# Kernel optimization log

Hardware: AMD Instinct MI355X
Metric: run time of the kernel (lower is better)

## Reference

```python
import jax, jax.numpy as jnp
import numpy as np

DIM = 128
HEADS = 4
DIM_HEAD = 32
NUM_MEM = 4
H = 256
W = 256
SCALE = DIM_HEAD ** -0.5
NORM_SCALE = DIM ** 0.5


def rms_norm(x, gamma):
    # x: (c, h, w); L2-normalize over channel axis, per spatial location
    x32 = x.astype(jnp.float32)
    n = jnp.linalg.norm(x32, ord=2, axis=0)  # (h, w)
    return (x32 / n * (gamma + 1.0) * NORM_SCALE).astype(x.dtype)


def setup_inputs() -> dict:
    key = jax.random.key(0)
    k0, k1, k2, k3 = jax.random.split(key, 4)
    x = jax.random.normal(k0, (DIM, H, W), dtype=jnp.float32)
    gamma1 = jnp.zeros((DIM, 1, 1), dtype=jnp.float32)
    w_qkv = jax.random.normal(k1, (3 * HEADS * DIM_HEAD, DIM), dtype=jnp.float32) * 0.05
    mem_kv = jax.random.normal(k2, (2, HEADS, DIM_HEAD, NUM_MEM), dtype=jnp.float32)
    w_out = jax.random.normal(k3, (DIM, HEADS * DIM_HEAD), dtype=jnp.float32) * 0.05
    b_out = jnp.zeros((DIM,), dtype=jnp.float32)
    gamma2 = jnp.zeros((DIM, 1, 1), dtype=jnp.float32)
    return {"x": x, "gamma1": gamma1, "w_qkv": w_qkv, "mem_kv": mem_kv,
            "w_out": w_out, "b_out": b_out, "gamma2": gamma2}


def reference(x, gamma1, w_qkv, mem_kv, w_out, b_out, gamma2):
    n = H * W
    xn = rms_norm(x, gamma1)
    # 1x1 conv == channel matmul: (3*hid, c) @ (c, h*w)
    qkv = jnp.einsum('oc,cn->on', w_qkv, xn.reshape(DIM, n))
    q, k, v = jnp.split(qkv, 3, axis=0)
    # (h*d, n) -> (h, d, n)
    q = q.reshape(HEADS, DIM_HEAD, n)
    k = k.reshape(HEADS, DIM_HEAD, n)
    v = v.reshape(HEADS, DIM_HEAD, n)
    mk, mv = mem_kv[0], mem_kv[1]  # (h, d, num_mem)
    k = jnp.concatenate([mk, k], axis=-1)  # (h, d, num_mem + n)
    v = jnp.concatenate([mv, v], axis=-1)
    # softmax over feature dim for q (global max subtract), token dim for k
    q = jax.nn.softmax((q - jnp.max(q)).astype(jnp.float32), axis=-2).astype(q.dtype)
    k = jax.nn.softmax((k - jnp.max(k)).astype(jnp.float32), axis=-1).astype(k.dtype)
    q = q * SCALE
    context = jnp.einsum('hdn,hen->hde', k, v)      # (h, d, d)
    out = jnp.einsum('hde,hdn->hen', context, q)    # (h, d, n)
    out = out.reshape(HEADS * DIM_HEAD, H, W)
    out = jnp.einsum('oc,chw->ohw', w_out, out) + b_out[:, None, None]
    return rms_norm(out, gamma2)
```

## Files before the change

### kernel.cpp

```cpp
#include <hip/hip_runtime.h>
#include <hip/hip_bf16.h>
#include <cstddef>


typedef __attribute__((ext_vector_type(8))) short short8;
typedef __attribute__((ext_vector_type(4))) float f32x4;

static constexpr int   NTOK = 65536;
static constexpr float NORM_SCALE_F = 11.313708498984761f;
static constexpr float SCALE_F      = 0.17677669529663687f;

__device__ __forceinline__ unsigned short f2bf(float f) {
  __hip_bfloat16 h = __float2bfloat16(f);
  return *reinterpret_cast<unsigned short*>(&h);
}

__global__ __launch_bounds__(256) void k0_pack(const float* __restrict__ w_qkv,
                                               const float* __restrict__ gamma1,
                                               unsigned short* __restrict__ Wp) {
  const int id = blockIdx.x * 256 + threadIdx.x;
  const int m = id / 16384, p = id % 16384;
  const int j = p & 7, ln = (p >> 3) & 63, frag = p >> 9;
  const int ks = frag & 3, rt = frag >> 2;
  const int row = rt * 16 + (ln & 15);
  const int c = ks * 32 + (ln >> 4) * 8 + j;
  const float v = w_qkv[(m * 128 + row) * 128 + c] * (gamma1[c] + 1.0f) * NORM_SCALE_F;
  Wp[id] = f2bf(v);
}

__global__ __launch_bounds__(512) void k1_kv(const float* __restrict__ x,
                                             const unsigned short* __restrict__ Wkp,
                                             const unsigned short* __restrict__ Wvp,
                                             float* __restrict__ Cp,
                                             float* __restrict__ Sp) {
  __shared__ unsigned short kvs[8][2560];
  const int tid = threadIdx.x, wv = tid >> 6, ln = tid & 63;
  const int g4 = ln >> 4, t16 = ln & 15;
  const int n0 = (blockIdx.x * 8 + wv) * 32;
  unsigned short* keb = &kvs[wv][0];
  unsigned short* vb  = &kvs[wv][1280];

  short8 xf[2][4];
  float scn[2];
  #pragma unroll
  for (int tg = 0; tg < 2; ++tg) {
    float sq = 0.f;
    #pragma unroll
    for (int ks = 0; ks < 4; ++ks) {
      short8 v;
      #pragma unroll
      for (int j = 0; j < 8; ++j) {
        const float f = x[(size_t)(ks * 32 + g4 * 8 + j) * NTOK + n0 + tg * 16 + t16];
        sq += f * f;
        v[j] = (short)f2bf(f);
      }
      xf[tg][ks] = v;
    }
    sq += __shfl_xor(sq, 16, 64);
    sq += __shfl_xor(sq, 32, 64);
    scn[tg] = rsqrtf(sq);
  }

  f32x4 cacc[4][2][2] = {};
  float sacc[4][2][4] = {};

  #pragma unroll
  for (int h = 0; h < 4; ++h) {
    f32x4 ka[2][2] = {};
    #pragma unroll
    for (int ks = 0; ks < 4; ++ks) {
      const short8 a0 = *reinterpret_cast<const short8*>(Wkp + (((2 * h + 0) * 4 + ks) * 64 + ln) * 8);
      const short8 a1 = *reinterpret_cast<const short8*>(Wkp + (((2 * h + 1) * 4 + ks) * 64 + ln) * 8);
      #pragma unroll
      for (int tg = 0; tg < 2; ++tg) {
        ka[0][tg] = __builtin_amdgcn_mfma_f32_16x16x32_bf16(a0, xf[tg][ks], ka[0][tg], 0, 0, 0);
        ka[1][tg] = __builtin_amdgcn_mfma_f32_16x16x32_bf16(a1, xf[tg][ks], ka[1][tg], 0, 0, 0);
      }
    }
    #pragma unroll
    for (int rtl = 0; rtl < 2; ++rtl)
      #pragma unroll
      for (int tg = 0; tg < 2; ++tg)
        #pragma unroll
        for (int r = 0; r < 4; ++r) {
          const float ke = __expf(ka[rtl][tg][r] * scn[tg]);
          sacc[h][rtl][r] += ke;
          keb[(rtl * 16 + g4 * 4 + r) * 40 + tg * 16 + t16] = f2bf(ke);
        }
    f32x4 va[2][2] = {};
    #pragma unroll
    for (int ks = 0; ks < 4; ++ks) {
      const short8 a0 = *reinterpret_cast<const short8*>(Wvp + (((2 * h + 0) * 4 + ks) * 64 + ln) * 8);
      const short8 a1 = *reinterpret_cast<const short8*>(Wvp + (((2 * h + 1) * 4 + ks) * 64 + ln) * 8);
      #pragma unroll
      for (int tg = 0; tg < 2; ++tg) {
        va[0][tg] = __builtin_amdgcn_mfma_f32_16x16x32_bf16(a0, xf[tg][ks], va[0][tg], 0, 0, 0);
        va[1][tg] = __builtin_amdgcn_mfma_f32_16x16x32_bf16(a1, xf[tg][ks], va[1][tg], 0, 0, 0);
      }
    }
    #pragma unroll
    for (int rtl = 0; rtl < 2; ++rtl)
      #pragma unroll
      for (int tg = 0; tg < 2; ++tg)
        #pragma unroll
        for (int r = 0; r < 4; ++r)
          vb[(rtl * 16 + g4 * 4 + r) * 40 + tg * 16 + t16] = f2bf(va[rtl][tg][r] * scn[tg]);

    asm volatile("s_waitcnt lgkmcnt(0)" ::: "memory");
    short8 keA[2], vB[2];
    #pragma unroll
    for (int dt = 0; dt < 2; ++dt)
      keA[dt] = *reinterpret_cast<const short8*>(keb + (dt * 16 + t16) * 40 + g4 * 8);
    #pragma unroll
    for (int et = 0; et < 2; ++et)
      vB[et] = *reinterpret_cast<const short8*>(vb + (et * 16 + t16) * 40 + g4 * 8);
    #pragma unroll
    for (int dt = 0; dt < 2; ++dt)
      #pragma unroll
      for (int et = 0; et < 2; ++et)
        cacc[h][dt][et] = __builtin_amdgcn_mfma_f32_16x16x32_bf16(keA[dt], vB[et], cacc[h][dt][et], 0, 0, 0);
    asm volatile("s_waitcnt lgkmcnt(0)" ::: "memory");
  }

  #pragma unroll
  for (int h = 0; h < 4; ++h)
    #pragma unroll
    for (int rtl = 0; rtl < 2; ++rtl)
      #pragma unroll
      for (int r = 0; r < 4; ++r) {
        float s = sacc[h][rtl][r];
        s += __shfl_xor(s, 1, 64);
        s += __shfl_xor(s, 2, 64);
        s += __shfl_xor(s, 4, 64);
        s += __shfl_xor(s, 8, 64);
        sacc[h][rtl][r] = s;
      }

  __syncthreads();
  float* cred = reinterpret_cast<float*>(&kvs[0][0]);
  for (int w = 0; w < 8; ++w) {
    if (wv == w) {
      #pragma unroll
      for (int h = 0; h < 4; ++h)
        #pragma unroll
        for (int dt = 0; dt < 2; ++dt)
          #pragma unroll
          for (int et = 0; et < 2; ++et)
            #pragma unroll
            for (int r = 0; r < 4; ++r) {
              const int idx = h * 1024 + (dt * 16 + g4 * 4 + r) * 32 + et * 16 + t16;
              if (w == 0) cred[idx] = cacc[h][dt][et][r];
              else        cred[idx] += cacc[h][dt][et][r];
            }
      if (t16 == 0) {
        #pragma unroll
        for (int h = 0; h < 4; ++h)
          #pragma unroll
          for (int rtl = 0; rtl < 2; ++rtl)
            #pragma unroll
            for (int r = 0; r < 4; ++r) {
              const int si = 4096 + h * 32 + rtl * 16 + g4 * 4 + r;
              if (w == 0) cred[si] = sacc[h][rtl][r];
              else        cred[si] += sacc[h][rtl][r];
            }
      }
    }
    __syncthreads();
  }
  for (int i = tid; i < 4096; i += 512)
    Cp[(size_t)blockIdx.x * 4096 + i] = cred[i];
  if (tid < 128)
    Sp[blockIdx.x * 128 + tid] = cred[4096 + tid];
}

__global__ __launch_bounds__(256) void k3a_reduce(const float* __restrict__ Cp,
                                                  const float* __restrict__ Sp,
                                                  float* __restrict__ Cpp) {
  __shared__ float red[256];
  const int t = threadIdx.x;
  const int eg = blockIdx.x;
  const int ch = blockIdx.y;
  const int e = eg * 128 + (t & 127);
  const int half = t >> 7;
  float s = 0.f;
  for (int bb = 0; bb < 16; ++bb) {
    const int b = ch * 32 + half * 16 + bb;
    s += (e < 4096) ? Cp[(size_t)b * 4096 + e] : Sp[b * 128 + (e - 4096)];
  }
  red[t] = s;
  __syncthreads();
  if (t < 128) Cpp[ch * 4224 + eg * 128 + t] = red[t] + red[t + 128];
}

__global__ __launch_bounds__(256) void k3b1_ctx(const float* __restrict__ Cpp,
                                                const float* __restrict__ mem_kv,
                                                float* __restrict__ ctx) {
  __shared__ float allv[4224];
  const int t = threadIdx.x;
  for (int e = t; e < 4224; e += 256) {
    float s = 0.f;
    #pragma unroll
    for (int c = 0; c < 8; ++c) s += Cpp[c * 4224 + e];
    allv[e] = s;
  }
  __syncthreads();
  for (int e = t; e < 4224; e += 256) {
    if (e < 4096) {
      const int hh = e >> 10, d = (e >> 5) & 31, ev = e & 31;
      float add = 0.f;
      #pragma unroll
      for (int m = 0; m < 4; ++m)
        add += __expf(mem_kv[(hh * 32 + d) * 4 + m]) * mem_kv[512 + (hh * 32 + ev) * 4 + m];
      allv[e] += add;
    } else {
      const int si = e - 4096;
      const int hh = si >> 5, d = si & 31;
      float add = 0.f;
      #pragma unroll
      for (int m = 0; m < 4; ++m) add += __expf(mem_kv[(hh * 32 + d) * 4 + m]);
      allv[e] += add;
    }
  }
  __syncthreads();
  for (int e = t; e < 4096; e += 256)
    ctx[e] = allv[e] / allv[4096 + (e >> 5)];
}

__global__ __launch_bounds__(256) void k3b2_w2(const float* __restrict__ ctx,
                                               const float* __restrict__ w_out,
                                               unsigned short* __restrict__ W2p) {
  const int t = threadIdx.x;
  const int hd = t & 127;
  const int og = t >> 7;
  const int hh = hd >> 5, d = hd & 31;
  const int bo = blockIdx.x;
  #pragma unroll
  for (int i = 0; i < 8; ++i) {
    const int o = bo * 16 + og * 8 + i;
    float s = 0.f;
    #pragma unroll
    for (int e = 0; e < 32; ++e)
      s += w_out[o * 128 + hh * 32 + e] * ctx[hh * 1024 + d * 32 + e];
    const int rt = o >> 4, ks = hd >> 5;
    const int lnp = ((hd & 31) >> 3) * 16 + (o & 15);
    const int j = hd & 7;
    W2p[((rt * 4 + ks) * 64 + lnp) * 8 + j] = f2bf(s * SCALE_F);
  }
}

__global__ __launch_bounds__(512) void k5_out(const float* __restrict__ x,
                                              const unsigned short* __restrict__ Wqp,
                                              const unsigned short* __restrict__ W2p,
                                              const float* __restrict__ b_out,
                                              const float* __restrict__ gamma2,
                                              float* __restrict__ y) {
  __shared__ unsigned short qs[8][4096];
  const int tid = threadIdx.x, wv = tid >> 6, ln = tid & 63;
  const int g4 = ln >> 4, t16 = ln & 15;
  const int n0 = (blockIdx.x * 8 + wv) * 32;
  unsigned short* qb_lds = &qs[wv][0];

  short8 xf[2][4];
  float scn[2];
  #pragma unroll
  for (int tg = 0; tg < 2; ++tg) {
    float sq = 0.f;
    #pragma unroll
    for (int ks = 0; ks < 4; ++ks) {
      short8 v;
      #pragma unroll
      for (int j = 0; j < 8; ++j) {
        const float f = x[(size_t)(ks * 32 + g4 * 8 + j) * NTOK + n0 + tg * 16 + t16];
        sq += f * f;
        v[j] = (short)f2bf(f);
      }
      xf[tg][ks] = v;
    }
    sq += __shfl_xor(sq, 16, 64);
    sq += __shfl_xor(sq, 32, 64);
    scn[tg] = rsqrtf(sq);
  }

  #pragma unroll
  for (int h = 0; h < 4; ++h) {
    f32x4 qa[2][2] = {};
    #pragma unroll
    for (int ks = 0; ks < 4; ++ks) {
      const short8 a0 = *reinterpret_cast<const short8*>(Wqp + (((2 * h + 0) * 4 + ks) * 64 + ln) * 8);
      const short8 a1 = *reinterpret_cast<const short8*>(Wqp + (((2 * h + 1) * 4 + ks) * 64 + ln) * 8);
      #pragma unroll
      for (int tg = 0; tg < 2; ++tg) {
        qa[0][tg] = __builtin_amdgcn_mfma_f32_16x16x32_bf16(a0, xf[tg][ks], qa[0][tg], 0, 0, 0);
        qa[1][tg] = __builtin_amdgcn_mfma_f32_16x16x32_bf16(a1, xf[tg][ks], qa[1][tg], 0, 0, 0);
      }
    }
    #pragma unroll
    for (int tg = 0; tg < 2; ++tg) {
      float ev[2][4];
      float s = 0.f;
      #pragma unroll
      for (int rtl = 0; rtl < 2; ++rtl)
        #pragma unroll
        for (int r = 0; r < 4; ++r) {
          ev[rtl][r] = __expf(qa[rtl][tg][r] * scn[tg]);
          s += ev[rtl][r];
        }
      s += __shfl_xor(s, 16, 64);
      s += __shfl_xor(s, 32, 64);
      const float inv = 1.0f / s;
      #pragma unroll
      for (int rtl = 0; rtl < 2; ++rtl)
        #pragma unroll
        for (int r = 0; r < 4; ++r)
          qa[rtl][tg][r] = ev[rtl][r] * inv;
    }
    #pragma unroll
    for (int rtl = 0; rtl < 2; ++rtl) {
      const int rt = 2 * h + rtl;
      #pragma unroll
      for (int tg = 0; tg < 2; ++tg) {
        ushort4 w4;
        w4.x = f2bf(qa[rtl][tg][0]);
        w4.y = f2bf(qa[rtl][tg][1]);
        w4.z = f2bf(qa[rtl][tg][2]);
        w4.w = f2bf(qa[rtl][tg][3]);
        const int idxb = ((tg * 4 + (rt >> 1)) * 64 + ((rt & 1) * 2 + (g4 >> 1)) * 16 + t16) * 8 + (g4 & 1) * 4;
        *reinterpret_cast<ushort4*>(&qb_lds[idxb]) = w4;
      }
    }
  }

  asm volatile("s_waitcnt lgkmcnt(0)" ::: "memory");

  short8 qb[2][4];
  #pragma unroll
  for (int tg = 0; tg < 2; ++tg)
    #pragma unroll
    for (int ks = 0; ks < 4; ++ks)
      qb[tg][ks] = *reinterpret_cast<const short8*>(&qb_lds[((tg * 4 + ks) * 64 + ln) * 8]);

  f32x4 z[8][2] = {};
  #pragma unroll
  for (int ks = 0; ks < 4; ++ks)
    #pragma unroll
    for (int rt = 0; rt < 8; ++rt) {
      const short8 a = *reinterpret_cast<const short8*>(W2p + ((rt * 4 + ks) * 64 + ln) * 8);
      #pragma unroll
      for (int tg = 0; tg < 2; ++tg)
        z[rt][tg] = __builtin_amdgcn_mfma_f32_16x16x32_bf16(a, qb[tg][ks], z[rt][tg], 0, 0, 0);
    }

  float ssq[2] = {0.f, 0.f};
  #pragma unroll
  for (int rt = 0; rt < 8; ++rt) {
    const float4 bb = *reinterpret_cast<const float4*>(b_out + rt * 16 + g4 * 4);
    const float barr[4] = {bb.x, bb.y, bb.z, bb.w};
    #pragma unroll
    for (int tg = 0; tg < 2; ++tg)
      #pragma unroll
      for (int r = 0; r < 4; ++r) {
        const float zb = z[rt][tg][r] + barr[r];
        z[rt][tg][r] = zb;
        ssq[tg] += zb * zb;
      }
  }
  float rr[2];
  #pragma unroll
  for (int tg = 0; tg < 2; ++tg) {
    float s = ssq[tg];
    s += __shfl_xor(s, 16, 64);
    s += __shfl_xor(s, 32, 64);
    rr[tg] = rsqrtf(s);
  }
  #pragma unroll
  for (int rt = 0; rt < 8; ++rt) {
    const float4 gg = *reinterpret_cast<const float4*>(gamma2 + rt * 16 + g4 * 4);
    const float garr[4] = {gg.x, gg.y, gg.z, gg.w};
    #pragma unroll
    for (int tg = 0; tg < 2; ++tg)
      #pragma unroll
      for (int r = 0; r < 4; ++r) {
        const int row = rt * 16 + g4 * 4 + r;
        y[(size_t)row * NTOK + n0 + tg * 16 + t16] =
            z[rt][tg][r] * rr[tg] * (garr[r] + 1.0f) * NORM_SCALE_F;
      }
  }
}

extern "C" void kernel_launch(void* const* d_in, const int* in_sizes, int n_in,
                              void* d_out, int out_size, void* d_ws, size_t ws_size,
                              hipStream_t stream) {
  const float* x      = (const float*)d_in[0];
  const float* gamma1 = (const float*)d_in[1];
  const float* w_qkv  = (const float*)d_in[2];
  const float* mem_kv = (const float*)d_in[3];
  const float* w_out  = (const float*)d_in[4];
  const float* b_out  = (const float*)d_in[5];
  const float* gamma2 = (const float*)d_in[6];
  float* out = (float*)d_out;
  float* ws  = (float*)d_ws;

  unsigned short* Wqp = (unsigned short*)ws;
  unsigned short* Wkp = Wqp + 16384;
  unsigned short* Wvp = Wkp + 16384;
  unsigned short* W2p = Wvp + 16384;
  float* Cp  = ws + 32768;
  float* Sp  = Cp + 1048576;
  float* Cpp = Sp + 32768;
  float* ctx = Cpp + 33792;

  hipLaunchKernelGGL(k0_pack,  dim3(192),    dim3(256), 0, stream, w_qkv, gamma1, Wqp);
  hipLaunchKernelGGL(k1_kv,    dim3(256),    dim3(512), 0, stream, x, Wkp, Wvp, Cp, Sp);
  hipLaunchKernelGGL(k3a_reduce, dim3(33, 8), dim3(256), 0, stream, Cp, Sp, Cpp);
  hipLaunchKernelGGL(k3b1_ctx, dim3(1),      dim3(256), 0, stream, Cpp, mem_kv, ctx);
  hipLaunchKernelGGL(k3b2_w2,  dim3(8),      dim3(256), 0, stream, ctx, w_out, W2p);
  hipLaunchKernelGGL(k5_out,   dim3(256),    dim3(512), 0, stream, x, Wqp, W2p, b_out, gamma2, out);
}
```

Measured before the change: 204.4 us.

## Swap MFMA operand roles to keep K/V and Q fragments in registers

Swaps the MFMA operand order so the projected K, V and Q tiles come out in the register layout needed as inputs to the next MFMA. This drops the per-wave LDS staging round-trips in both the kv and output kernels. The x normalization moves before the bf16 conversion. Per-block reductions of context and sums now use shared-memory atomics into one combined buffer instead of a serialized per-wave loop. The output kernel is relaunched with 256-thread blocks and no LDS, and the W2 packing writes vectorized fragments. In exchange there is atomic contention on LDS, and applying the norm scale before rounding slightly changes the numerics.

```diff
diff --git a/kernel.cpp b/kernel.cpp
--- a/kernel.cpp
+++ b/kernel.cpp
@@ -14,6 +14,7 @@
   __hip_bfloat16 h = __float2bfloat16(f);
   return *reinterpret_cast<unsigned short*>(&h);
 }
+__device__ __forceinline__ short sbf(float f) { return (short)f2bf(f); }
 
 __global__ __launch_bounds__(256) void k0_pack(const float* __restrict__ w_qkv,
                                                const float* __restrict__ gamma1,
@@ -31,150 +32,111 @@
 __global__ __launch_bounds__(512) void k1_kv(const float* __restrict__ x,
                                              const unsigned short* __restrict__ Wkp,
                                              const unsigned short* __restrict__ Wvp,
-                                             float* __restrict__ Cp,
-                                             float* __restrict__ Sp) {
-  __shared__ unsigned short kvs[8][2560];
+                                             float* __restrict__ CpAll) {
+  __shared__ float cred[4224];
   const int tid = threadIdx.x, wv = tid >> 6, ln = tid & 63;
   const int g4 = ln >> 4, t16 = ln & 15;
   const int n0 = (blockIdx.x * 8 + wv) * 32;
-  unsigned short* keb = &kvs[wv][0];
-  unsigned short* vb  = &kvs[wv][1280];
+
+  for (int i = tid; i < 4224; i += 512) cred[i] = 0.f;
+  __syncthreads();
 
   short8 xf[2][4];
-  float scn[2];
   #pragma unroll
   for (int tg = 0; tg < 2; ++tg) {
+    float tmp[4][8];
     float sq = 0.f;
     #pragma unroll
-    for (int ks = 0; ks < 4; ++ks) {
-      short8 v;
+    for (int ks = 0; ks < 4; ++ks)
       #pragma unroll
       for (int j = 0; j < 8; ++j) {
         const float f = x[(size_t)(ks * 32 + g4 * 8 + j) * NTOK + n0 + tg * 16 + t16];
+        tmp[ks][j] = f;
         sq += f * f;
-        v[j] = (short)f2bf(f);
-      }
-      xf[tg][ks] = v;
-    }
+      }
     sq += __shfl_xor(sq, 16, 64);
     sq += __shfl_xor(sq, 32, 64);
-    scn[tg] = rsqrtf(sq);
-  }
-
-  f32x4 cacc[4][2][2] = {};
-  float sacc[4][2][4] = {};
+    const float s = rsqrtf(sq);
+    #pragma unroll
+    for (int ks = 0; ks < 4; ++ks) {
+      short8 v;
+      #pragma unroll
+      for (int j = 0; j < 8; ++j) v[j] = sbf(tmp[ks][j] * s);
+      xf[tg][ks] = v;
+    }
+  }
 
   #pragma unroll
   for (int h = 0; h < 4; ++h) {
     f32x4 ka[2][2] = {};
     #pragma unroll
     for (int ks = 0; ks < 4; ++ks) {
-      const short8 a0 = *reinterpret_cast<const short8*>(Wkp + (((2 * h + 0) * 4 + ks) * 64 + ln) * 8);
-      const short8 a1 = *reinterpret_cast<const short8*>(Wkp + (((2 * h + 1) * 4 + ks) * 64 + ln) * 8);
+      const short8 b0 = *reinterpret_cast<const short8*>(Wkp + (((2 * h + 0) * 4 + ks) * 64 + ln) * 8);
+      const short8 b1 = *reinterpret_cast<const short8*>(Wkp + (((2 * h + 1) * 4 + ks) * 64 + ln) * 8);
       #pragma unroll
       for (int tg = 0; tg < 2; ++tg) {
-        ka[0][tg] = __builtin_amdgcn_mfma_f32_16x16x32_bf16(a0, xf[tg][ks], ka[0][tg], 0, 0, 0);
-        ka[1][tg] = __builtin_amdgcn_mfma_f32_16x16x32_bf16(a1, xf[tg][ks], ka[1][tg], 0, 0, 0);
-      }
-    }
-    #pragma unroll
-    for (int rtl = 0; rtl < 2; ++rtl)
+        ka[0][tg] = __builtin_amdgcn_mfma_f32_16x16x32_bf16(xf[tg][ks], b0, ka[0][tg], 0, 0, 0);
+        ka[1][tg] = __builtin_amdgcn_mfma_f32_16x16x32_bf16(xf[tg][ks], b1, ka[1][tg], 0, 0, 0);
+      }
+    }
+    short8 keA[2];
+    #pragma unroll
+    for (int mt = 0; mt < 2; ++mt) {
+      float sl = 0.f;
+      short8 u;
       #pragma unroll
       for (int tg = 0; tg < 2; ++tg)
         #pragma unroll
         for (int r = 0; r < 4; ++r) {
-          const float ke = __expf(ka[rtl][tg][r] * scn[tg]);
-          sacc[h][rtl][r] += ke;
-          keb[(rtl * 16 + g4 * 4 + r) * 40 + tg * 16 + t16] = f2bf(ke);
+          const float e = __expf(ka[mt][tg][r]);
+          sl += e;
+          u[tg * 4 + r] = sbf(e);
         }
+      keA[mt] = u;
+      sl += __shfl_xor(sl, 16, 64);
+      sl += __shfl_xor(sl, 32, 64);
+      if (g4 == 0) atomicAdd(&cred[4096 + h * 32 + mt * 16 + t16], sl);
+    }
     f32x4 va[2][2] = {};
     #pragma unroll
     for (int ks = 0; ks < 4; ++ks) {
-      const short8 a0 = *reinterpret_cast<const short8*>(Wvp + (((2 * h + 0) * 4 + ks) * 64 + ln) * 8);
-      const short8 a1 = *reinterpret_cast<const short8*>(Wvp + (((2 * h + 1) * 4 + ks) * 64 + ln) * 8);
+      const short8 b0 = *reinterpret_cast<const short8*>(Wvp + (((2 * h + 0) * 4 + ks) * 64 + ln) * 8);
+      const short8 b1 = *reinterpret_cast<const short8*>(Wvp + (((2 * h + 1) * 4 + ks) * 64 + ln) * 8);
       #pragma unroll
       for (int tg = 0; tg < 2; ++tg) {
-        va[0][tg] = __builtin_amdgcn_mfma_f32_16x16x32_bf16(a0, xf[tg][ks], va[0][tg], 0, 0, 0);
-        va[1][tg] = __builtin_amdgcn_mfma_f32_16x16x32_bf16(a1, xf[tg][ks], va[1][tg], 0, 0, 0);
-      }
-    }
-    #pragma unroll
-    for (int rtl = 0; rtl < 2; ++rtl)
+        va[0][tg] = __builtin_amdgcn_mfma_f32_16x16x32_bf16(xf[tg][ks], b0, va[0][tg], 0, 0, 0);
+        va[1][tg] = __builtin_amdgcn_mfma_f32_16x16x32_bf16(xf[tg][ks], b1, va[1][tg], 0, 0, 0);
+      }
+    }
+    short8 vB[2];
+    #pragma unroll
+    for (int et = 0; et < 2; ++et) {
+      short8 u;
       #pragma unroll
       for (int tg = 0; tg < 2; ++tg)
         #pragma unroll
         for (int r = 0; r < 4; ++r)
-          vb[(rtl * 16 + g4 * 4 + r) * 40 + tg * 16 + t16] = f2bf(va[rtl][tg][r] * scn[tg]);
-
-    asm volatile("s_waitcnt lgkmcnt(0)" ::: "memory");
-    short8 keA[2], vB[2];
+          u[tg * 4 + r] = sbf(va[et][tg][r]);
+      vB[et] = u;
+    }
     #pragma unroll
     for (int dt = 0; dt < 2; ++dt)
-      keA[dt] = *reinterpret_cast<const short8*>(keb + (dt * 16 + t16) * 40 + g4 * 8);
-    #pragma unroll
-    for (int et = 0; et < 2; ++et)
-      vB[et] = *reinterpret_cast<const short8*>(vb + (et * 16 + t16) * 40 + g4 * 8);
-    #pragma unroll
-    for (int dt = 0; dt < 2; ++dt)
-      #pragma unroll
-      for (int et = 0; et < 2; ++et)
-        cacc[h][dt][et] = __builtin_amdgcn_mfma_f32_16x16x32_bf16(keA[dt], vB[et], cacc[h][dt][et], 0, 0, 0);
-    asm volatile("s_waitcnt lgkmcnt(0)" ::: "memory");
-  }
-
-  #pragma unroll
-  for (int h = 0; h < 4; ++h)
-    #pragma unroll
-    for (int rtl = 0; rtl < 2; ++rtl)
-      #pragma unroll
-      for (int r = 0; r < 4; ++r) {
-        float s = sacc[h][rtl][r];
-        s += __shfl_xor(s, 1, 64);
-        s += __shfl_xor(s, 2, 64);
-        s += __shfl_xor(s, 4, 64);
-        s += __shfl_xor(s, 8, 64);
-        sacc[h][rtl][r] = s;
-      }
-
-  __syncthreads();
-  float* cred = reinterpret_cast<float*>(&kvs[0][0]);
-  for (int w = 0; w < 8; ++w) {
-    if (wv == w) {
-      #pragma unroll
-      for (int h = 0; h < 4; ++h)
-        #pragma unroll
-        for (int dt = 0; dt < 2; ++dt)
-          #pragma unroll
-          for (int et = 0; et < 2; ++et)
-            #pragma unroll
-            for (int r = 0; r < 4; ++r) {
-              const int idx = h * 1024 + (dt * 16 + g4 * 4 + r) * 32 + et * 16 + t16;
-              if (w == 0) cred[idx] = cacc[h][dt][et][r];
-              else        cred[idx] += cacc[h][dt][et][r];
-            }
-      if (t16 == 0) {
-        #pragma unroll
-        for (int h = 0; h < 4; ++h)
-          #pragma unroll
-          for (int rtl = 0; rtl < 2; ++rtl)
-            #pragma unroll
-            for (int r = 0; r < 4; ++r) {
-              const int si = 4096 + h * 32 + rtl * 16 + g4 * 4 + r;
-              if (w == 0) cred[si] = sacc[h][rtl][r];
-              else        cred[si] += sacc[h][rtl][r];
-            }
-      }
-    }
-    __syncthreads();
-  }
-  for (int i = tid; i < 4096; i += 512)
-    Cp[(size_t)blockIdx.x * 4096 + i] = cred[i];
-  if (tid < 128)
-    Sp[blockIdx.x * 128 + tid] = cred[4096 + tid];
-}
-
-__global__ __launch_bounds__(256) void k3a_reduce(const float* __restrict__ Cp,
-                                                  const float* __restrict__ Sp,
+      #pragma unroll
+      for (int et = 0; et < 2; ++et) {
+        f32x4 zc = {0.f, 0.f, 0.f, 0.f};
+        zc = __builtin_amdgcn_mfma_f32_16x16x32_bf16(keA[dt], vB[et], zc, 0, 0, 0);
+        #pragma unroll
+        for (int r = 0; r < 4; ++r)
+          atomicAdd(&cred[h * 1024 + (dt * 16 + g4 * 4 + r) * 32 + et * 16 + t16], zc[r]);
+      }
+  }
+
+  __syncthreads();
+  for (int i = tid; i < 4224; i += 512)
+    CpAll[(size_t)blockIdx.x * 4224 + i] = cred[i];
+}
+
+__global__ __launch_bounds__(256) void k3a_reduce(const float* __restrict__ CpAll,
                                                   float* __restrict__ Cpp) {
   __shared__ float red[256];
   const int t = threadIdx.x;
@@ -185,7 +147,7 @@
   float s = 0.f;
   for (int bb = 0; bb < 16; ++bb) {
     const int b = ch * 32 + half * 16 + bb;
-    s += (e < 4096) ? Cp[(size_t)b * 4096 + e] : Sp[b * 128 + (e - 4096)];
+    s += CpAll[(size_t)b * 4224 + e];
   }
   red[t] = s;
   __syncthreads();
@@ -229,58 +191,63 @@
 __global__ __launch_bounds__(256) void k3b2_w2(const float* __restrict__ ctx,
                                                const float* __restrict__ w_out,
                                                unsigned short* __restrict__ W2p) {
-  const int t = threadIdx.x;
-  const int hd = t & 127;
-  const int og = t >> 7;
-  const int hh = hd >> 5, d = hd & 31;
-  const int bo = blockIdx.x;
-  #pragma unroll
-  for (int i = 0; i < 8; ++i) {
-    const int o = bo * 16 + og * 8 + i;
+  const int base = (blockIdx.x * 256 + threadIdx.x) * 8;
+  const int ln = (base >> 3) & 63;
+  const int frag = base >> 9;
+  const int h = frag & 3, ot = frag >> 2;
+  const int o = ot * 16 + (ln & 15);
+  float wrow[32];
+  #pragma unroll
+  for (int e = 0; e < 32; ++e) wrow[e] = w_out[o * 128 + h * 32 + e];
+  short8 out8;
+  #pragma unroll
+  for (int j = 0; j < 8; ++j) {
+    const int d = (j >> 2) * 16 + ((ln >> 4) << 2) + (j & 3);
     float s = 0.f;
     #pragma unroll
     for (int e = 0; e < 32; ++e)
-      s += w_out[o * 128 + hh * 32 + e] * ctx[hh * 1024 + d * 32 + e];
-    const int rt = o >> 4, ks = hd >> 5;
-    const int lnp = ((hd & 31) >> 3) * 16 + (o & 15);
-    const int j = hd & 7;
-    W2p[((rt * 4 + ks) * 64 + lnp) * 8 + j] = f2bf(s * SCALE_F);
-  }
-}
-
-__global__ __launch_bounds__(512) void k5_out(const float* __restrict__ x,
+      s += wrow[e] * ctx[h * 1024 + d * 32 + e];
+    out8[j] = sbf(s * SCALE_F);
+  }
+  *reinterpret_cast<short8*>(W2p + base) = out8;
+}
+
+__global__ __launch_bounds__(256) void k5_out(const float* __restrict__ x,
                                               const unsigned short* __restrict__ Wqp,
                                               const unsigned short* __restrict__ W2p,
                                               const float* __restrict__ b_out,
                                               const float* __restrict__ gamma2,
                                               float* __restrict__ y) {
-  __shared__ unsigned short qs[8][4096];
   const int tid = threadIdx.x, wv = tid >> 6, ln = tid & 63;
   const int g4 = ln >> 4, t16 = ln & 15;
-  const int n0 = (blockIdx.x * 8 + wv) * 32;
-  unsigned short* qb_lds = &qs[wv][0];
+  const int n0 = (blockIdx.x * 4 + wv) * 32;
 
   short8 xf[2][4];
-  float scn[2];
   #pragma unroll
   for (int tg = 0; tg < 2; ++tg) {
+    float tmp[4][8];
     float sq = 0.f;
     #pragma unroll
-    for (int ks = 0; ks < 4; ++ks) {
-      short8 v;
+    for (int ks = 0; ks < 4; ++ks)
       #pragma unroll
       for (int j = 0; j < 8; ++j) {
         const float f = x[(size_t)(ks * 32 + g4 * 8 + j) * NTOK + n0 + tg * 16 + t16];
+        tmp[ks][j] = f;
         sq += f * f;
-        v[j] = (short)f2bf(f);
-      }
-      xf[tg][ks] = v;
-    }
+      }
     sq += __shfl_xor(sq, 16, 64);
     sq += __shfl_xor(sq, 32, 64);
-    scn[tg] = rsqrtf(sq);
-  }
-
+    const float s = rsqrtf(sq);
+    #pragma unroll
+    for (int ks = 0; ks < 4; ++ks) {
+      short8 v;
+      #pragma unroll
+      for (int j = 0; j < 8; ++j) v[j] = sbf(tmp[ks][j] * s);
+      xf[tg][ks] = v;
+    }
+  }
+
+  short8 qB[4][2];
   #pragma unroll
   for (int h = 0; h < 4; ++h) {
     f32x4 qa[2][2] = {};
@@ -297,70 +264,49 @@
     #pragma unroll
     for (int tg = 0; tg < 2; ++tg) {
       float ev[2][4];
-      float s = 0.f;
+      float ss = 0.f;
       #pragma unroll
       for (int rtl = 0; rtl < 2; ++rtl)
         #pragma unroll
         for (int r = 0; r < 4; ++r) {
-          ev[rtl][r] = __expf(qa[rtl][tg][r] * scn[tg]);
-          s += ev[rtl][r];
+          ev[rtl][r] = __expf(qa[rtl][tg][r]);
+          ss += ev[rtl][r];
         }
-      s += __shfl_xor(s, 16, 64);
-      s += __shfl_xor(s, 32, 64);
-      const float inv = 1.0f / s;
+      ss += __shfl_xor(ss, 16, 64);
+      ss += __shfl_xor(ss, 32, 64);
+      const float inv = 1.0f / ss;
+      short8 u;
       #pragma unroll
       for (int rtl = 0; rtl < 2; ++rtl)
         #pragma unroll
         for (int r = 0; r < 4; ++r)
-          qa[rtl][tg][r] = ev[rtl][r] * inv;
-    }
-    #pragma unroll
-    for (int rtl = 0; rtl < 2; ++rtl) {
-      const int rt = 2 * h + rtl;
-      #pragma unroll
-      for (int tg = 0; tg < 2; ++tg) {
-        ushort4 w4;
-        w4.x = f2bf(qa[rtl][tg][0]);
-        w4.y = f2bf(qa[rtl][tg][1]);
-        w4.z = f2bf(qa[rtl][tg][2]);
-        w4.w = f2bf(qa[rtl][tg][3]);
-        const int idxb = ((tg * 4 + (rt >> 1)) * 64 + ((rt & 1) * 2 + (g4 >> 1)) * 16 + t16) * 8 + (g4 & 1) * 4;
-        *reinterpret_cast<ushort4*>(&qb_lds[idxb]) = w4;
-      }
-    }
-  }
-
-  asm volatile("s_waitcnt lgkmcnt(0)" ::: "memory");
-
-  short8 qb[2][4];
-  #pragma unroll
-  for (int tg = 0; tg < 2; ++tg)
-    #pragma unroll
-    for (int ks = 0; ks < 4; ++ks)
-      qb[tg][ks] = *reinterpret_cast<const short8*>(&qb_lds[((tg * 4 + ks) * 64 + ln) * 8]);
+          u[rtl * 4 + r] = sbf(ev[rtl][r] * inv);
+      qB[h][tg] = u;
+    }
+  }
 
   f32x4 z[8][2] = {};
   #pragma unroll
-  for (int ks = 0; ks < 4; ++ks)
-    #pragma unroll
-    for (int rt = 0; rt < 8; ++rt) {
-      const short8 a = *reinterpret_cast<const short8*>(W2p + ((rt * 4 + ks) * 64 + ln) * 8);
+  for (int h = 0; h < 4; ++h)
+    #pragma unroll
+    for (int ot = 0; ot < 8; ++ot) {
+      const short8 a = *reinterpret_cast<const short8*>(W2p + ((ot * 4 + h) * 64 + ln) * 8);
       #pragma unroll
       for (int tg = 0; tg < 2; ++tg)
-        z[rt][tg] = __builtin_amdgcn_mfma_f32_16x16x32_bf16(a, qb[tg][ks], z[rt][tg], 0, 0, 0);
+        z[ot][tg] = __builtin_amdgcn_mfma_f32_16x16x32_bf16(a, qB[h][tg], z[ot][tg], 0, 0, 0);
     }
 
   float ssq[2] = {0.f, 0.f};
   #pragma unroll
-  for (int rt = 0; rt < 8; ++rt) {
-    const float4 bb = *reinterpret_cast<const float4*>(b_out + rt * 16 + g4 * 4);
+  for (int ot = 0; ot < 8; ++ot) {
+    const float4 bb = *reinterpret_cast<const float4*>(b_out + ot * 16 + g4 * 4);
     const float barr[4] = {bb.x, bb.y, bb.z, bb.w};
     #pragma unroll
     for (int tg = 0; tg < 2; ++tg)
       #pragma unroll
       for (int r = 0; r < 4; ++r) {
-        const float zb = z[rt][tg][r] + barr[r];
-        z[rt][tg][r] = zb;
+        const float zb = z[ot][tg][r] + barr[r];
+        z[ot][tg][r] = zb;
         ssq[tg] += zb * zb;
       }
   }
@@ -373,16 +319,16 @@
     rr[tg] = rsqrtf(s);
   }
   #pragma unroll
-  for (int rt = 0; rt < 8; ++rt) {
-    const float4 gg = *reinterpret_cast<const float4*>(gamma2 + rt * 16 + g4 * 4);
+  for (int ot = 0; ot < 8; ++ot) {
+    const float4 gg = *reinterpret_cast<const float4*>(gamma2 + ot * 16 + g4 * 4);
     const float garr[4] = {gg.x, gg.y, gg.z, gg.w};
     #pragma unroll
     for (int tg = 0; tg < 2; ++tg)
       #pragma unroll
       for (int r = 0; r < 4; ++r) {
-        const int row = rt * 16 + g4 * 4 + r;
+        const int row = ot * 16 + g4 * 4 + r;
         y[(size_t)row * NTOK + n0 + tg * 16 + t16] =
-            z[rt][tg][r] * rr[tg] * (garr[r] + 1.0f) * NORM_SCALE_F;
+            z[ot][tg][r] * rr[tg] * (garr[r] + 1.0f) * NORM_SCALE_F;
       }
   }
 }
@@ -404,15 +350,14 @@
   unsigned short* Wkp = Wqp + 16384;
   unsigned short* Wvp = Wkp + 16384;
   unsigned short* W2p = Wvp + 16384;
-  float* Cp  = ws + 32768;
-  float* Sp  = Cp + 1048576;
-  float* Cpp = Sp + 32768;
-  float* ctx = Cpp + 33792;
-
-  hipLaunchKernelGGL(k0_pack,  dim3(192),    dim3(256), 0, stream, w_qkv, gamma1, Wqp);
-  hipLaunchKernelGGL(k1_kv,    dim3(256),    dim3(512), 0, stream, x, Wkp, Wvp, Cp, Sp);
-  hipLaunchKernelGGL(k3a_reduce, dim3(33, 8), dim3(256), 0, stream, Cp, Sp, Cpp);
-  hipLaunchKernelGGL(k3b1_ctx, dim3(1),      dim3(256), 0, stream, Cpp, mem_kv, ctx);
-  hipLaunchKernelGGL(k3b2_w2,  dim3(8),      dim3(256), 0, stream, ctx, w_out, W2p);
-  hipLaunchKernelGGL(k5_out,   dim3(256),    dim3(512), 0, stream, x, Wqp, W2p, b_out, gamma2, out);
-}
+  float* CpAll = ws + 32768;
+  float* Cpp   = CpAll + 1081344;
+  float* ctx   = Cpp + 33792;
+
+  hipLaunchKernelGGL(k0_pack,    dim3(192),    dim3(256), 0, stream, w_qkv, gamma1, Wqp);
+  hipLaunchKernelGGL(k1_kv,      dim3(256),    dim3(512), 0, stream, x, Wkp, Wvp, CpAll);
+  hipLaunchKernelGGL(k3a_reduce, dim3(33, 8),  dim3(256), 0, stream, CpAll, Cpp);
+  hipLaunchKernelGGL(k3b1_ctx,   dim3(1),      dim3(256), 0, stream, Cpp, mem_kv, ctx);
+  hipLaunchKernelGGL(k3b2_w2,    dim3(8),      dim3(256), 0, stream, ctx, w_out, W2p);
+  hipLaunchKernelGGL(k5_out,     dim3(512),    dim3(256), 0, stream, x, Wqp, W2p, b_out, gamma2, out);
+}
```

Result: faster. 173.5 us (-15.1%).
